# Kernel tuning notes

Measured on AMD Instinct MI355X. Metric: run time of the kernel, lower is better.

The kernel has to match this reference:

```python
import jax, jax.numpy as jnp
import numpy as np

EPS = 1e-6
NUM_HEADS = 16


def _layernorm(x, g, b):
    m = jnp.mean(x, axis=-1, keepdims=True)
    v = jnp.mean(jnp.square(x - m), axis=-1, keepdims=True)
    return (x - m) / jnp.sqrt(v + EPS) * g + b


def _rotate_half(x):
    x1, x2 = jnp.split(x, 2, axis=-1)
    return jnp.concatenate([-x2, x1], axis=-1)


def setup_inputs() -> dict:
    key = jax.random.key(0)
    B, N, C = 2, 2048, 1024
    H = NUM_HEADS
    D = C // H
    F = int(C * 4.0)
    ks = jax.random.split(key, 12)
    s = 0.02
    pos = jnp.arange(N)[:, None].astype(jnp.float32)
    inv_freq = 1.0 / (10000.0 ** (jnp.arange(0, D, 2, dtype=jnp.float32) / D))
    freqs = pos * inv_freq[None, :]          # [N, D/2]
    emb = jnp.concatenate([freqs, freqs], axis=-1)  # [N, D]
    return {
        "x": jax.random.normal(ks[0], (B, N, C), jnp.float32),
        "rotary_cos": jnp.cos(emb),
        "rotary_sin": jnp.sin(emb),
        "ln1_g": jnp.ones((C,), jnp.float32),
        "ln1_b": jnp.zeros((C,), jnp.float32),
        "Wq": jax.random.normal(ks[1], (C, C), jnp.float32) * s,
        "bq": jnp.zeros((C,), jnp.float32),
        "Wk": jax.random.normal(ks[2], (C, C), jnp.float32) * s,
        "bk": jnp.zeros((C,), jnp.float32),
        "Wv": jax.random.normal(ks[3], (C, C), jnp.float32) * s,
        "bv": jnp.zeros((C,), jnp.float32),
        "Wo": jax.random.normal(ks[4], (C, C), jnp.float32) * s,
        "bo": jnp.zeros((C,), jnp.float32),
        "ln2_g": jnp.ones((C,), jnp.float32),
        "ln2_b": jnp.zeros((C,), jnp.float32),
        "W1": jax.random.normal(ks[5], (F, C), jnp.float32) * s,
        "b1": jnp.zeros((F,), jnp.float32),
        "W2": jax.random.normal(ks[6], (C, F), jnp.float32) * s,
        "b2": jnp.zeros((C,), jnp.float32),
    }


def reference(x, rotary_cos, rotary_sin, ln1_g, ln1_b, Wq, bq, Wk, bk, Wv, bv,
              Wo, bo, ln2_g, ln2_b, W1, b1, W2, b2):
    B, N, C = x.shape
    H = NUM_HEADS
    D = C // H

    # --- attention branch ---
    h = _layernorm(x, ln1_g, ln1_b)
    q = (h @ Wq.T + bq).reshape(B, N, H, D).transpose(0, 2, 1, 3)  # [B,H,N,D]
    k = (h @ Wk.T + bk).reshape(B, N, H, D).transpose(0, 2, 1, 3)
    v = (h @ Wv.T + bv).reshape(B, N, H, D).transpose(0, 2, 1, 3)

    cos = rotary_cos[None, None, :, :]  # [1,1,N,D]
    sin = rotary_sin[None, None, :, :]
    q = q * cos + _rotate_half(q) * sin
    k = k * cos + _rotate_half(k) * sin

    scale = D ** -0.5
    attn = jnp.einsum('bhnd,bhmd->bhnm', q, k) * scale
    attn = jax.nn.softmax(attn, axis=-1)
    out = jnp.einsum('bhnm,bhmd->bhnd', attn, v)
    out = out.transpose(0, 2, 1, 3).reshape(B, N, C)
    out = out @ Wo.T + bo
    x = x + out

    # --- MLP branch ---
    h = _layernorm(x, ln2_g, ln2_b)
    h = jax.nn.gelu(h @ W1.T + b1, approximate=False)  # torch nn.GELU exact
    h = h @ W2.T + b2
    return x + h
```

## Files before the change

kernel.cpp:

```cpp
#include <hip/hip_runtime.h>
#include <hip/hip_bf16.h>

#define B_ 2
#define N_ 2048
#define C_ 1024
#define H_ 16
#define D_ 64
#define F_ 4096
#define M_ 4096

typedef __attribute__((ext_vector_type(8))) short bf16x8;
typedef __attribute__((ext_vector_type(4))) float f32x4;

__device__ inline unsigned short f2bf(float f) {
  unsigned int u = __float_as_uint(f);
  u = (u + 0x7FFFu + ((u >> 16) & 1u)) >> 16;
  return (unsigned short)u;
}
__device__ inline float bf2f(unsigned short u) {
  unsigned int x = ((unsigned int)u) << 16;
  return __uint_as_float(x);
}

__global__ __launch_bounds__(256)
void cvt_all(const float4* __restrict__ s0, const float4* __restrict__ s1,
             const float4* __restrict__ s2, const float4* __restrict__ s3,
             const float4* __restrict__ s4, const float4* __restrict__ s5,
             ushort4* __restrict__ d0, ushort4* __restrict__ d1,
             ushort4* __restrict__ d2, ushort4* __restrict__ d3,
             ushort4* __restrict__ d4, ushort4* __restrict__ d5) {
  int b = blockIdx.x;
  const float4* s; ushort4* d; int i;
  if      (b < 1024) { s = s0; d = d0; i = b * 256 + threadIdx.x; }
  else if (b < 2048) { s = s1; d = d1; i = (b - 1024) * 256 + threadIdx.x; }
  else if (b < 3072) { s = s2; d = d2; i = (b - 2048) * 256 + threadIdx.x; }
  else if (b < 4096) { s = s3; d = d3; i = (b - 3072) * 256 + threadIdx.x; }
  else if (b < 8192) { s = s4; d = d4; i = (b - 4096) * 256 + threadIdx.x; }
  else               { s = s5; d = d5; i = (b - 8192) * 256 + threadIdx.x; }
  float4 f = s[i];
  ushort4 o;
  o.x = f2bf(f.x); o.y = f2bf(f.y); o.z = f2bf(f.z); o.w = f2bf(f.w);
  d[i] = o;
}

__global__ __launch_bounds__(256)
void ln_kernel(const float* __restrict__ x, const float* __restrict__ g,
               const float* __restrict__ b, unsigned short* __restrict__ out) {
  __shared__ float red[8];
  const int row = blockIdx.x;
  const int t = threadIdx.x;
  const float4 xv = *(const float4*)(x + row * 1024 + t * 4);
  float s  = xv.x + xv.y + xv.z + xv.w;
  float sq = xv.x * xv.x + xv.y * xv.y + xv.z * xv.z + xv.w * xv.w;
  #pragma unroll
  for (int off = 32; off >= 1; off >>= 1) {
    s  += __shfl_down(s, off);
    sq += __shfl_down(sq, off);
  }
  const int lane = t & 63, wave = t >> 6;
  if (lane == 0) { red[wave * 2] = s; red[wave * 2 + 1] = sq; }
  __syncthreads();
  float ts = red[0] + red[2] + red[4] + red[6];
  float tq = red[1] + red[3] + red[5] + red[7];
  float mean = ts * (1.0f / 1024.0f);
  float var  = tq * (1.0f / 1024.0f) - mean * mean;
  float rstd = rsqrtf(var + 1e-6f);
  float xs[4] = {xv.x, xv.y, xv.z, xv.w};
  #pragma unroll
  for (int i = 0; i < 4; i++) {
    int c = t * 4 + i;
    float y = (xs[i] - mean) * rstd * g[c] + b[c];
    out[row * 1024 + c] = f2bf(y);
  }
}

template<int MODE, int BN>
__global__ __launch_bounds__(256)
void gemm_bt(const unsigned short* __restrict__ A,
             const unsigned short* __restrict__ Bw,
             int K, int Nout, int npc,
             const float* __restrict__ bias,
             const float* __restrict__ resid,
             unsigned short* __restrict__ out_bf,
             float* __restrict__ out_f32) {
  constexpr int NJ = BN / 32;
  __shared__ unsigned short sA[2][128 * 64];
  __shared__ unsigned short sB[2][BN * 64];
  const int t = threadIdx.x;
  const int wave = t >> 6, lane = t & 63;
  const int quad = lane >> 4, l16 = lane & 15;
  const int wm = (wave & 1) * 64, wn = (wave >> 1) * (BN / 2);
  const int id = blockIdx.y * gridDim.x + blockIdx.x;
  const int xcd = id & 7, r_ = id >> 3;
  const int m_blk = xcd * 4 + (r_ & 3);
  const int n_blk = r_ >> 2;
  const int m0 = m_blk * 128, n0 = n_blk * BN;

  f32x4 acc[4][NJ];
  #pragma unroll
  for (int i = 0; i < 4; i++)
    #pragma unroll
    for (int j = 0; j < NJ; j++) acc[i][j] = (f32x4){0.f, 0.f, 0.f, 0.f};

  const int sc = (((t & 7) ^ ((t >> 3) & 7)) * 8);
  const unsigned short* gA = A  + (m0 + (t >> 3)) * K + sc;
  const unsigned short* gB = Bw + (n0 + (t >> 3)) * K + sc;

  auto stage = [&](int k0, int buf) {
    unsigned short* lA = &sA[buf][(wave * 8) * 64];
    unsigned short* lB = &sB[buf][(wave * 8) * 64];
    #pragma unroll
    for (int i = 0; i < 4; i++)
      __builtin_amdgcn_global_load_lds((const unsigned int*)(gA + (32 * i) * K + k0),
                                       (unsigned int*)(lA + 32 * i * 64), 16, 0, 0);
    #pragma unroll
    for (int i = 0; i < BN / 32; i++)
      __builtin_amdgcn_global_load_lds((const unsigned int*)(gB + (32 * i) * K + k0),
                                       (unsigned int*)(lB + 32 * i * 64), 16, 0, 0);
  };

  stage(0, 0);
  __syncthreads();

  const int so0 = ((quad ^ (l16 & 7)) * 8);
  const int so1 = (((4 + quad) ^ (l16 & 7)) * 8);

  const int nk = K >> 6;
  for (int kt = 0; kt < nk; kt++) {
    const int cur = kt & 1;
    if (kt + 1 < nk) stage((kt + 1) * 64, cur ^ 1);
    #pragma unroll
    for (int kk = 0; kk < 2; kk++) {
      const int so = kk ? so1 : so0;
      bf16x8 af[4], bfr[NJ];
      #pragma unroll
      for (int i = 0; i < 4; i++)
        af[i] = *(const bf16x8*)(&sA[cur][(wm + i * 16 + l16) * 64 + so]);
      #pragma unroll
      for (int j = 0; j < NJ; j++)
        bfr[j] = *(const bf16x8*)(&sB[cur][(wn + j * 16 + l16) * 64 + so]);
      #pragma unroll
      for (int i = 0; i < 4; i++)
        #pragma unroll
        for (int j = 0; j < NJ; j++)
          acc[i][j] = __builtin_amdgcn_mfma_f32_16x16x32_bf16(af[i], bfr[j], acc[i][j], 0, 0, 0);
    }
    __syncthreads();
  }

  #pragma unroll
  for (int i = 0; i < 4; i++) {
    #pragma unroll
    for (int j = 0; j < NJ; j++) {
      int col = n0 + wn + j * 16 + l16;
      #pragma unroll
      for (int r = 0; r < 4; r++) {
        int row = m0 + wm + i * 16 + quad * 4 + r;
        float v = acc[i][j][r];
        if (MODE == 1 || MODE == 3) {
          out_f32[row * Nout + col] = v + bias[col] + resid[row * Nout + col];
        } else {
          v += bias[col];
          float w = v * (1.0f + 0.044715f * v * v);
          float gl = v / (1.0f + __expf(-1.5957691216f * w));
          out_bf[row * Nout + col] = f2bf(gl);
        }
      }
    }
  }
}

template<int EPI>
__global__ __launch_bounds__(512, 1)
void gemm256(const unsigned short* __restrict__ A,
             const unsigned short* __restrict__ Bw,
             const float* __restrict__ bias,
             const float* __restrict__ bq, const float* __restrict__ bk,
             const float* __restrict__ bv,
             const float* __restrict__ rc, const float* __restrict__ rs,
             unsigned short* __restrict__ o0,
             unsigned short* __restrict__ ko, unsigned short* __restrict__ vt) {
  const int K = 1024;
  __shared__ unsigned short sA[2][256 * 64];
  __shared__ unsigned short sB[2][256 * 64];
  const int t = threadIdx.x;
  const int wave = t >> 6, lane = t & 63;
  const int quad = lane >> 4, l16 = lane & 15;
  const int wm = (wave & 1) * 128, wn = (wave >> 1) * 64;
  const int id = blockIdx.x;
  const int xcd = id & 7, r_ = id >> 3;
  int m_blk, n_blk;
  if (EPI == 0) { n_blk = xcd * 2 + (r_ >> 4); m_blk = r_ & 15; }
  else          { m_blk = xcd * 2 + r_ / 12;   n_blk = r_ % 12; }
  const int m0 = m_blk * 256, n0 = n_blk * 256;

  f32x4 acc[8][4];
  #pragma unroll
  for (int i = 0; i < 8; i++)
    #pragma unroll
    for (int j = 0; j < 4; j++) acc[i][j] = (f32x4){0.f, 0.f, 0.f, 0.f};

  const int sc = (((t & 7) ^ ((t >> 3) & 7)) * 8);
  const unsigned short* gA = A  + (m0 + (t >> 3)) * K + sc;
  const unsigned short* gB = Bw + (n0 + (t >> 3)) * K + sc;

  auto stage_pair = [&](int k0, int buf, int pr) {
    if (pr < 2) {
      unsigned short* lA = &sA[buf][(wave * 8) * 64];
      #pragma unroll
      for (int r = pr * 2; r < pr * 2 + 2; r++)
        __builtin_amdgcn_global_load_lds((const unsigned int*)(gA + (64 * r) * K + k0),
                                         (unsigned int*)(lA + 64 * r * 64), 16, 0, 0);
    } else {
      unsigned short* lB = &sB[buf][(wave * 8) * 64];
      #pragma unroll
      for (int r = (pr - 2) * 2; r < (pr - 2) * 2 + 2; r++)
        __builtin_amdgcn_global_load_lds((const unsigned int*)(gB + (64 * r) * K + k0),
                                         (unsigned int*)(lB + 64 * r * 64), 16, 0, 0);
    }
  };

  stage_pair(0, 0, 0); stage_pair(0, 0, 1); stage_pair(0, 0, 2); stage_pair(0, 0, 3);
  stage_pair(64, 1, 0);
  asm volatile("s_waitcnt vmcnt(2)" ::: "memory");
  __builtin_amdgcn_s_barrier();

  const int so0 = ((quad ^ (l16 & 7)) * 8);
  const int so1 = (((4 + quad) ^ (l16 & 7)) * 8);

  const int nk = K >> 6;
  for (int t_ = 0; t_ < nk; t_++) {
    const int R = t_ & 1;
    const unsigned short* rA = sA[R];
    const unsigned short* rB = sB[R];
    #pragma unroll
    for (int p = 0; p < 4; p++) {
      const int kk = p >> 1, ih = p & 1;
      const int so = kk ? so1 : so0;
      bf16x8 af[4], bfr[4];
      #pragma unroll
      for (int ii = 0; ii < 4; ii++)
        af[ii] = *(const bf16x8*)(&rA[(wm + (ih * 4 + ii) * 16 + l16) * 64 + so]);
      #pragma unroll
      for (int j = 0; j < 4; j++)
        bfr[j] = *(const bf16x8*)(&rB[(wn + j * 16 + l16) * 64 + so]);
      if (p < 3 && t_ + 1 < nk) stage_pair((t_ + 1) * 64, R ^ 1, p + 1);
      __builtin_amdgcn_s_barrier();
      asm volatile("s_waitcnt lgkmcnt(0)" ::: "memory");
      __builtin_amdgcn_sched_barrier(0);
      __builtin_amdgcn_s_setprio(1);
      #pragma unroll
      for (int ii = 0; ii < 4; ii++)
        #pragma unroll
        for (int j = 0; j < 4; j++)
          acc[ih * 4 + ii][j] =
              __builtin_amdgcn_mfma_f32_16x16x32_bf16(af[ii], bfr[j], acc[ih * 4 + ii][j], 0, 0, 0);
      __builtin_amdgcn_s_setprio(0);
      if (p < 3) __builtin_amdgcn_s_barrier();
    }
    __builtin_amdgcn_s_barrier();
    if (t_ + 2 < nk) {
      stage_pair((t_ + 2) * 64, R, 0);
      asm volatile("s_waitcnt vmcnt(2)" ::: "memory");
      __builtin_amdgcn_s_barrier();
    } else if (t_ + 1 < nk) {
      asm volatile("s_waitcnt vmcnt(0)" ::: "memory");
      __builtin_amdgcn_s_barrier();
    }
  }

  if (EPI == 0) {
    #pragma unroll
    for (int i = 0; i < 8; i++) {
      #pragma unroll
      for (int j = 0; j < 4; j++) {
        int col = n0 + wn + j * 16 + l16;
        float bb = bias[col];
        #pragma unroll
        for (int r = 0; r < 4; r++) {
          int row = m0 + wm + i * 16 + quad * 4 + r;
          float v = acc[i][j][r] + bb;
          float w = v * (1.0f + 0.044715f * v * v);
          float gl = v / (1.0f + __expf(-1.5957691216f * w));
          o0[row * 4096 + col] = f2bf(gl);
        }
      }
    }
  } else {
    const int rgn = n_blk >> 2;
    const int c0 = (n_blk & 3) * 256;
    if (rgn == 2) {
      #pragma unroll
      for (int i = 0; i < 8; i++) {
        int row0 = m0 + wm + i * 16 + quad * 4;
        int bidx = row0 >> 11, n0r = row0 & 2047;
        #pragma unroll
        for (int j = 0; j < 4; j++) {
          int d = j * 16 + l16;
          int c = c0 + wn + d;
          int h = c >> 6;
          float bb = bv[c];
          __hip_bfloat162 p01 = __float22bfloat162_rn(float2{acc[i][j][0] + bb, acc[i][j][1] + bb});
          __hip_bfloat162 p23 = __float22bfloat162_rn(float2{acc[i][j][2] + bb, acc[i][j][3] + bb});
          unsigned int u01, u23;
          __builtin_memcpy(&u01, &p01, 4);
          __builtin_memcpy(&u23, &p23, 4);
          *(uint2*)(vt + (((bidx * 16 + h) * 64) + d) * 2048 + n0r) = make_uint2(u01, u23);
        }
      }
    } else {
      const float* bia = (rgn == 0) ? bq : bk;
      unsigned short* outp = (rgn == 0) ? o0 : ko;
      #pragma unroll
      for (int i = 0; i < 8; i++) {
        #pragma unroll
        for (int r = 0; r < 4; r++) {
          int row = m0 + wm + i * 16 + quad * 4 + r;
          int bidx = row >> 11, n = row & 2047;
          #pragma unroll
          for (int j = 0; j < 4; j++) {
            int d = j * 16 + l16;
            int c = c0 + wn + d;
            int h = c >> 6;
            int oi = ((bidx * 16 + h) * 2048 + n) * 64 + d;
            float val = acc[i][j][r] + bia[c];
            float pv  = acc[i][j ^ 2][r] + bia[c ^ 32];
            float rot = (j < 2) ? -pv : pv;
            float y = val * rc[n * 64 + d] + rot * rs[n * 64 + d];
            if (rgn == 0) y *= 0.125f;
            outp[oi] = f2bf(y);
          }
        }
      }
    }
  }
}

__global__ __launch_bounds__(512)
void flash_attn(const unsigned short* __restrict__ q,
                const unsigned short* __restrict__ k,
                const unsigned short* __restrict__ vt,
                unsigned short* __restrict__ o0h,
                unsigned short* __restrict__ o1h,
                float* __restrict__ l0g, float* __restrict__ l1g) {
  __shared__ unsigned short sK[2][64 * 64];
  __shared__ unsigned short sVt[2][64 * 64];
  __shared__ unsigned short sPt[2][8][16 * 72];
  const int t = threadIdx.x;
  const int wave = t >> 6, lane = t & 63;
  const int quad = lane >> 4, l16 = lane & 15;
  const int id = blockIdx.x;
  const int bh = (id & 7) * 4 + ((id >> 3) & 3);
  const int qb = (id >> 5) & 7;
  const int kvh = id >> 8;
  const int base = bh * (N_ * D_);

  bf16x8 qa[2][2];
  #pragma unroll
  for (int qt = 0; qt < 2; qt++) {
    int qrow = qb * 256 + wave * 32 + qt * 16 + l16;
    #pragma unroll
    for (int kk = 0; kk < 2; kk++)
      qa[qt][kk] = *(const bf16x8*)(q + base + qrow * D_ + kk * 32 + quad * 8);
  }
  float l_i[2] = {0.f, 0.f};
  f32x4 o_acc[2][4];
  #pragma unroll
  for (int qt = 0; qt < 2; qt++)
    #pragma unroll
    for (int dt = 0; dt < 4; dt++) o_acc[qt][dt] = (f32x4){0.f, 0.f, 0.f, 0.f};

  const int sc = (((t & 7) ^ ((t >> 3) & 7)) * 8);
  const unsigned short* gK  = k  + base + (t >> 3) * 64 + sc;
  const unsigned short* gVt = vt + bh * (64 * 2048) + (t >> 3) * 2048 + sc;

  auto stage = [&](int kt, int buf) {
    __builtin_amdgcn_global_load_lds((const unsigned int*)(gK + kt * 64 * 64),
                                     (unsigned int*)(&sK[buf][(wave * 8) * 64]), 16, 0, 0);
    __builtin_amdgcn_global_load_lds((const unsigned int*)(gVt + kt * 64),
                                     (unsigned int*)(&sVt[buf][(wave * 8) * 64]), 16, 0, 0);
  };
  const int kt0 = kvh * 16, kt1 = kt0 + 16;
  stage(kt0, 0);
  __syncthreads();

  const int so0 = ((quad ^ (l16 & 7)) * 8);
  const int so1 = (((4 + quad) ^ (l16 & 7)) * 8);

  for (int kt = kt0; kt < kt1; kt++) {
    const int cur = kt & 1;
    if (kt + 1 < kt1) stage(kt + 1, cur ^ 1);

    f32x4 s_acc[2][4];
    #pragma unroll
    for (int nt = 0; nt < 4; nt++) {
      bf16x8 kb0 = *(const bf16x8*)(&sK[cur][(nt * 16 + l16) * 64 + so0]);
      bf16x8 kb1 = *(const bf16x8*)(&sK[cur][(nt * 16 + l16) * 64 + so1]);
      #pragma unroll
      for (int qt = 0; qt < 2; qt++) {
        f32x4 a = (f32x4){0.f, 0.f, 0.f, 0.f};
        a = __builtin_amdgcn_mfma_f32_16x16x32_bf16(kb0, qa[qt][0], a, 0, 0, 0);
        a = __builtin_amdgcn_mfma_f32_16x16x32_bf16(kb1, qa[qt][1], a, 0, 0, 0);
        s_acc[qt][nt] = a;
      }
    }
    #pragma unroll
    for (int qt = 0; qt < 2; qt++) {
      float rsum = 0.f;
      #pragma unroll
      for (int nt = 0; nt < 4; nt++)
        #pragma unroll
        for (int r = 0; r < 4; r++) {
          float p = __expf(s_acc[qt][nt][r]);
          s_acc[qt][nt][r] = p;
          rsum += p;
        }
      rsum += __shfl_xor(rsum, 16);
      rsum += __shfl_xor(rsum, 32);
      l_i[qt] += rsum;
      #pragma unroll
      for (int nt = 0; nt < 4; nt++) {
        __hip_bfloat162 p01 = __float22bfloat162_rn(float2{s_acc[qt][nt][0], s_acc[qt][nt][1]});
        __hip_bfloat162 p23 = __float22bfloat162_rn(float2{s_acc[qt][nt][2], s_acc[qt][nt][3]});
        unsigned int u01, u23;
        __builtin_memcpy(&u01, &p01, 4);
        __builtin_memcpy(&u23, &p23, 4);
        *(uint2*)(&sPt[qt][wave][l16 * 72 + nt * 16 + quad * 4]) = make_uint2(u01, u23);
      }
    }
    __asm__ volatile("s_waitcnt lgkmcnt(0)" ::: "memory");
    bf16x8 pt[2][2];
    #pragma unroll
    for (int qt = 0; qt < 2; qt++) {
      pt[qt][0] = *(const bf16x8*)(&sPt[qt][wave][l16 * 72 + quad * 8]);
      pt[qt][1] = *(const bf16x8*)(&sPt[qt][wave][l16 * 72 + 32 + quad * 8]);
    }
    #pragma unroll
    for (int dt = 0; dt < 4; dt++) {
      int d0 = dt * 16 + l16;
      bf16x8 va0 = *(const bf16x8*)(&sVt[cur][d0 * 64 + so0]);
      bf16x8 va1 = *(const bf16x8*)(&sVt[cur][d0 * 64 + so1]);
      #pragma unroll
      for (int qt = 0; qt < 2; qt++) {
        o_acc[qt][dt] = __builtin_amdgcn_mfma_f32_16x16x32_bf16(va0, pt[qt][0], o_acc[qt][dt], 0, 0, 0);
        o_acc[qt][dt] = __builtin_amdgcn_mfma_f32_16x16x32_bf16(va1, pt[qt][1], o_acc[qt][dt], 0, 0, 0);
      }
    }
    __syncthreads();
  }

  unsigned short* op = kvh ? o1h : o0h;
  float* lp = kvh ? l1g : l0g;
  const int b = bh >> 4, h = bh & 15;
  #pragma unroll
  for (int qt = 0; qt < 2; qt++) {
    const int qrow = qb * 256 + wave * 32 + qt * 16 + l16;
    if (quad == 0) lp[bh * 2048 + qrow] = l_i[qt];
    const int tok = b * N_ + qrow;
    #pragma unroll
    for (int dt = 0; dt < 4; dt++) {
      __hip_bfloat162 p01 = __float22bfloat162_rn(float2{o_acc[qt][dt][0], o_acc[qt][dt][1]});
      __hip_bfloat162 p23 = __float22bfloat162_rn(float2{o_acc[qt][dt][2], o_acc[qt][dt][3]});
      unsigned int u01, u23;
      __builtin_memcpy(&u01, &p01, 4);
      __builtin_memcpy(&u23, &p23, 4);
      int col = h * 64 + dt * 16 + quad * 4;
      *(uint2*)(op + tok * C_ + col) = make_uint2(u01, u23);
    }
  }
}

__global__ __launch_bounds__(256)
void attn_norm(const unsigned short* __restrict__ o0h,
               const unsigned short* __restrict__ o1h,
               const float* __restrict__ l0g, const float* __restrict__ l1g,
               unsigned short* __restrict__ o) {
  const int i = (blockIdx.x * 256 + threadIdx.x) * 8;
  const int row = i >> 10, c = i & 1023;
  const int h = c >> 6;
  const int b = row >> 11, n = row & 2047;
  const int li = (b * 16 + h) * 2048 + n;
  const float inv = 1.0f / (l0g[li] + l1g[li]);
  ushort4 a0 = *(const ushort4*)(o0h + i);
  ushort4 a1 = *(const ushort4*)(o0h + i + 4);
  ushort4 b0 = *(const ushort4*)(o1h + i);
  ushort4 b1 = *(const ushort4*)(o1h + i + 4);
  ushort4 r0, r1;
  r0.x = f2bf((bf2f(a0.x) + bf2f(b0.x)) * inv);
  r0.y = f2bf((bf2f(a0.y) + bf2f(b0.y)) * inv);
  r0.z = f2bf((bf2f(a0.z) + bf2f(b0.z)) * inv);
  r0.w = f2bf((bf2f(a0.w) + bf2f(b0.w)) * inv);
  r1.x = f2bf((bf2f(a1.x) + bf2f(b1.x)) * inv);
  r1.y = f2bf((bf2f(a1.y) + bf2f(b1.y)) * inv);
  r1.z = f2bf((bf2f(a1.z) + bf2f(b1.z)) * inv);
  r1.w = f2bf((bf2f(a1.w) + bf2f(b1.w)) * inv);
  *(ushort4*)(o + i) = r0;
  *(ushort4*)(o + i + 4) = r1;
}

extern "C" void kernel_launch(void* const* d_in, const int* in_sizes, int n_in,
                              void* d_out, int out_size, void* d_ws, size_t ws_size,
                              hipStream_t stream) {
  const float* x   = (const float*)d_in[0];
  const float* rc  = (const float*)d_in[1];
  const float* rs  = (const float*)d_in[2];
  const float* g1  = (const float*)d_in[3];
  const float* be1 = (const float*)d_in[4];
  const float* Wq  = (const float*)d_in[5];
  const float* bq  = (const float*)d_in[6];
  const float* Wk  = (const float*)d_in[7];
  const float* bk  = (const float*)d_in[8];
  const float* Wv  = (const float*)d_in[9];
  const float* bv  = (const float*)d_in[10];
  const float* Wo  = (const float*)d_in[11];
  const float* bo  = (const float*)d_in[12];
  const float* g2  = (const float*)d_in[13];
  const float* be2 = (const float*)d_in[14];
  const float* W1  = (const float*)d_in[15];
  const float* b1m = (const float*)d_in[16];
  const float* W2  = (const float*)d_in[17];
  const float* b2m = (const float*)d_in[18];
  float* out = (float*)d_out;

  char* ws = (char*)d_ws;
  unsigned short* wqkv = (unsigned short*)(ws + 0);
  unsigned short* wo   = (unsigned short*)(ws + 6291456);
  unsigned short* w1   = (unsigned short*)(ws + 8388608);
  unsigned short* w2   = (unsigned short*)(ws + 16777216);
  unsigned short* h1   = (unsigned short*)(ws + 25165824);
  unsigned short* qa   = (unsigned short*)(ws + 33554432);
  unsigned short* ka   = (unsigned short*)(ws + 41943040);
  unsigned short* va   = (unsigned short*)(ws + 50331648);
  unsigned short* ao   = (unsigned short*)(ws + 58720256);
  float*          x1   = (float*)(ws + 67108864);
  float*          l0   = (float*)(ws + 67108864);
  float*          l1   = l0 + 65536;
  unsigned short* u    = (unsigned short*)(ws + 33554432);

  cvt_all<<<12288, 256, 0, stream>>>(
      (const float4*)Wq, (const float4*)Wk, (const float4*)Wv, (const float4*)Wo,
      (const float4*)W1, (const float4*)W2,
      (ushort4*)wqkv, (ushort4*)(wqkv + 1048576), (ushort4*)(wqkv + 2097152),
      (ushort4*)wo, (ushort4*)w1, (ushort4*)w2);

  ln_kernel<<<4096, 256, 0, stream>>>(x, g1, be1, h1);
  gemm256<1><<<192, 512, 0, stream>>>(h1, wqkv, nullptr, bq, bk, bv, rc, rs, qa, ka, va);
  flash_attn<<<512, 512, 0, stream>>>(qa, ka, va, ao, h1, l0, l1);
  attn_norm<<<2048, 256, 0, stream>>>(ao, h1, l0, l1, ao);
  gemm_bt<1, 64><<<dim3(16, 32), 256, 0, stream>>>(ao, wo, 1024, 1024, 2, bo, x, nullptr, x1);
  ln_kernel<<<4096, 256, 0, stream>>>(x1, g2, be2, h1);
  gemm256<0><<<256, 512, 0, stream>>>(h1, w1, b1m, nullptr, nullptr, nullptr, nullptr, nullptr,
                                      u, nullptr, nullptr);
  gemm_bt<3, 64><<<dim3(16, 32), 256, 0, stream>>>(u, w2, 4096, 1024, 2, b2m, x1, nullptr, out);
}
```

Measured before the change: 375.6 us.

## Replace Wo and W2 GEMMs with split-K 256x128 GEMM using atomic accumulation

The 128x64-tile gemm_bt used for the Wo and W2 projections is replaced by a 256x128-tile, 512-thread split-K kernel. It has a finer-grained staged pipeline with explicit barriers, waitcnt and setprio, and writes results with float atomic adds into an output buffer. That buffer is pre-filled by a separate add_bias kernel holding residual plus bias. The aim is larger tiles for more data reuse and enough blocks to fill the GPU on the K=4096 GEMM. The cost is two extra elementwise launches, atomic traffic in the epilogue, and a summation order that is no longer deterministic.

```diff
diff --git a/kernel.cpp b/kernel.cpp
--- a/kernel.cpp
+++ b/kernel.cpp
@@ -74,97 +74,136 @@
   }
 }
 
-template<int MODE, int BN>
 __global__ __launch_bounds__(256)
-void gemm_bt(const unsigned short* __restrict__ A,
-             const unsigned short* __restrict__ Bw,
-             int K, int Nout, int npc,
-             const float* __restrict__ bias,
-             const float* __restrict__ resid,
-             unsigned short* __restrict__ out_bf,
-             float* __restrict__ out_f32) {
-  constexpr int NJ = BN / 32;
-  __shared__ unsigned short sA[2][128 * 64];
-  __shared__ unsigned short sB[2][BN * 64];
+void add_bias(const float* __restrict__ resid, const float* __restrict__ bias,
+              float* __restrict__ out) {
+  const int i = (blockIdx.x * 256 + threadIdx.x) * 4;
+  const int col = i & 1023;
+  float4 r = *(const float4*)(resid + i);
+  float4 b = *(const float4*)(bias + col);
+  float4 o;
+  o.x = r.x + b.x; o.y = r.y + b.y; o.z = r.z + b.z; o.w = r.w + b.w;
+  *(float4*)(out + i) = o;
+}
+
+__global__ __launch_bounds__(512, 1)
+void gemm_splitk(const unsigned short* __restrict__ A,
+                 const unsigned short* __restrict__ Bw,
+                 int Kfull, int ksplit,
+                 float* __restrict__ out) {
+  __shared__ unsigned short sA[2][256 * 64];
+  __shared__ unsigned short sB[2][128 * 64];
   const int t = threadIdx.x;
   const int wave = t >> 6, lane = t & 63;
   const int quad = lane >> 4, l16 = lane & 15;
-  const int wm = (wave & 1) * 64, wn = (wave >> 1) * (BN / 2);
-  const int id = blockIdx.y * gridDim.x + blockIdx.x;
+  const int wm = (wave >> 1) * 64, wn = (wave & 1) * 64;
+  const int id = blockIdx.x;
   const int xcd = id & 7, r_ = id >> 3;
-  const int m_blk = xcd * 4 + (r_ & 3);
-  const int n_blk = r_ >> 2;
-  const int m0 = m_blk * 128, n0 = n_blk * BN;
-
-  f32x4 acc[4][NJ];
+  const int m_blk = xcd * 2 + (r_ & 1);
+  const int cu = r_ >> 1;
+  const int n_blk = cu & 7;
+  const int split = cu >> 3;
+  const int m0 = m_blk * 256, n0 = n_blk * 128;
+  const int k0base = split * ksplit;
+
+  f32x4 acc[4][4];
   #pragma unroll
   for (int i = 0; i < 4; i++)
     #pragma unroll
-    for (int j = 0; j < NJ; j++) acc[i][j] = (f32x4){0.f, 0.f, 0.f, 0.f};
+    for (int j = 0; j < 4; j++) acc[i][j] = (f32x4){0.f, 0.f, 0.f, 0.f};
 
   const int sc = (((t & 7) ^ ((t >> 3) & 7)) * 8);
-  const unsigned short* gA = A  + (m0 + (t >> 3)) * K + sc;
-  const unsigned short* gB = Bw + (n0 + (t >> 3)) * K + sc;
-
-  auto stage = [&](int k0, int buf) {
-    unsigned short* lA = &sA[buf][(wave * 8) * 64];
-    unsigned short* lB = &sB[buf][(wave * 8) * 64];
-    #pragma unroll
-    for (int i = 0; i < 4; i++)
-      __builtin_amdgcn_global_load_lds((const unsigned int*)(gA + (32 * i) * K + k0),
-                                       (unsigned int*)(lA + 32 * i * 64), 16, 0, 0);
-    #pragma unroll
-    for (int i = 0; i < BN / 32; i++)
-      __builtin_amdgcn_global_load_lds((const unsigned int*)(gB + (32 * i) * K + k0),
-                                       (unsigned int*)(lB + 32 * i * 64), 16, 0, 0);
+  const unsigned short* gA = A  + (long)(m0 + (t >> 3)) * Kfull + k0base + sc;
+  const unsigned short* gB = Bw + (long)(n0 + (t >> 3)) * Kfull + k0base + sc;
+
+  auto stage_pair = [&](int k0, int buf, int pr) {
+    if (pr < 2) {
+      #pragma unroll
+      for (int i = pr * 2; i < pr * 2 + 2; i++)
+        __builtin_amdgcn_global_load_lds((const unsigned int*)(gA + (long)(64 * i) * Kfull + k0),
+                                         (unsigned int*)(&sA[buf][i * 4096 + wave * 8 * 64]), 16, 0, 0);
+    } else {
+      #pragma unroll
+      for (int i = 0; i < 2; i++)
+        __builtin_amdgcn_global_load_lds((const unsigned int*)(gB + (long)(64 * i) * Kfull + k0),
+                                         (unsigned int*)(&sB[buf][i * 4096 + wave * 8 * 64]), 16, 0, 0);
+    }
   };
 
-  stage(0, 0);
-  __syncthreads();
+  stage_pair(0, 0, 0); stage_pair(0, 0, 1); stage_pair(0, 0, 2);
+  stage_pair(64, 1, 0);
+  asm volatile("s_waitcnt vmcnt(2)" ::: "memory");
+  __builtin_amdgcn_s_barrier();
 
   const int so0 = ((quad ^ (l16 & 7)) * 8);
   const int so1 = (((4 + quad) ^ (l16 & 7)) * 8);
 
-  const int nk = K >> 6;
-  for (int kt = 0; kt < nk; kt++) {
-    const int cur = kt & 1;
-    if (kt + 1 < nk) stage((kt + 1) * 64, cur ^ 1);
-    #pragma unroll
-    for (int kk = 0; kk < 2; kk++) {
-      const int so = kk ? so1 : so0;
-      bf16x8 af[4], bfr[NJ];
-      #pragma unroll
-      for (int i = 0; i < 4; i++)
-        af[i] = *(const bf16x8*)(&sA[cur][(wm + i * 16 + l16) * 64 + so]);
-      #pragma unroll
-      for (int j = 0; j < NJ; j++)
-        bfr[j] = *(const bf16x8*)(&sB[cur][(wn + j * 16 + l16) * 64 + so]);
-      #pragma unroll
-      for (int i = 0; i < 4; i++)
-        #pragma unroll
-        for (int j = 0; j < NJ; j++)
-          acc[i][j] = __builtin_amdgcn_mfma_f32_16x16x32_bf16(af[i], bfr[j], acc[i][j], 0, 0, 0);
-    }
-    __syncthreads();
-  }
-
-  #pragma unroll
-  for (int i = 0; i < 4; i++) {
-    #pragma unroll
-    for (int j = 0; j < NJ; j++) {
+  const int nk = ksplit >> 6;
+  for (int t_ = 0; t_ < nk; t_++) {
+    const int R = t_ & 1;
+    const unsigned short* rA = sA[R];
+    const unsigned short* rB = sB[R];
+    {
+      bf16x8 af[4], bfr[4];
+      #pragma unroll
+      for (int ii = 0; ii < 4; ii++)
+        af[ii] = *(const bf16x8*)(&rA[(wm + ii * 16 + l16) * 64 + so0]);
+      #pragma unroll
+      for (int j = 0; j < 4; j++)
+        bfr[j] = *(const bf16x8*)(&rB[(wn + j * 16 + l16) * 64 + so0]);
+      if (t_ + 1 < nk) stage_pair((t_ + 1) * 64, R ^ 1, 1);
+      __builtin_amdgcn_s_barrier();
+      asm volatile("s_waitcnt lgkmcnt(0)" ::: "memory");
+      __builtin_amdgcn_sched_barrier(0);
+      __builtin_amdgcn_s_setprio(1);
+      #pragma unroll
+      for (int ii = 0; ii < 4; ii++)
+        #pragma unroll
+        for (int j = 0; j < 4; j++)
+          acc[ii][j] = __builtin_amdgcn_mfma_f32_16x16x32_bf16(af[ii], bfr[j], acc[ii][j], 0, 0, 0);
+      __builtin_amdgcn_s_setprio(0);
+      __builtin_amdgcn_s_barrier();
+    }
+    {
+      bf16x8 af[4], bfr[4];
+      #pragma unroll
+      for (int ii = 0; ii < 4; ii++)
+        af[ii] = *(const bf16x8*)(&rA[(wm + ii * 16 + l16) * 64 + so1]);
+      #pragma unroll
+      for (int j = 0; j < 4; j++)
+        bfr[j] = *(const bf16x8*)(&rB[(wn + j * 16 + l16) * 64 + so1]);
+      if (t_ + 1 < nk) stage_pair((t_ + 1) * 64, R ^ 1, 2);
+      __builtin_amdgcn_s_barrier();
+      asm volatile("s_waitcnt lgkmcnt(0)" ::: "memory");
+      __builtin_amdgcn_sched_barrier(0);
+      __builtin_amdgcn_s_setprio(1);
+      #pragma unroll
+      for (int ii = 0; ii < 4; ii++)
+        #pragma unroll
+        for (int j = 0; j < 4; j++)
+          acc[ii][j] = __builtin_amdgcn_mfma_f32_16x16x32_bf16(af[ii], bfr[j], acc[ii][j], 0, 0, 0);
+      __builtin_amdgcn_s_setprio(0);
+    }
+    __builtin_amdgcn_s_barrier();
+    if (t_ + 2 < nk) {
+      stage_pair((t_ + 2) * 64, R, 0);
+      asm volatile("s_waitcnt vmcnt(2)" ::: "memory");
+      __builtin_amdgcn_s_barrier();
+    } else if (t_ + 1 < nk) {
+      asm volatile("s_waitcnt vmcnt(0)" ::: "memory");
+      __builtin_amdgcn_s_barrier();
+    }
+  }
+
+  #pragma unroll
+  for (int ii = 0; ii < 4; ii++) {
+    #pragma unroll
+    for (int j = 0; j < 4; j++) {
       int col = n0 + wn + j * 16 + l16;
       #pragma unroll
       for (int r = 0; r < 4; r++) {
-        int row = m0 + wm + i * 16 + quad * 4 + r;
-        float v = acc[i][j][r];
-        if (MODE == 1 || MODE == 3) {
-          out_f32[row * Nout + col] = v + bias[col] + resid[row * Nout + col];
-        } else {
-          v += bias[col];
-          float w = v * (1.0f + 0.044715f * v * v);
-          float gl = v / (1.0f + __expf(-1.5957691216f * w));
-          out_bf[row * Nout + col] = f2bf(gl);
-        }
+        int row = m0 + wm + ii * 16 + quad * 4 + r;
+        unsafeAtomicAdd(&out[row * 1024 + col], acc[ii][j][r]);
       }
     }
   }
@@ -547,9 +586,11 @@
   gemm256<1><<<192, 512, 0, stream>>>(h1, wqkv, nullptr, bq, bk, bv, rc, rs, qa, ka, va);
   flash_attn<<<512, 512, 0, stream>>>(qa, ka, va, ao, h1, l0, l1);
   attn_norm<<<2048, 256, 0, stream>>>(ao, h1, l0, l1, ao);
-  gemm_bt<1, 64><<<dim3(16, 32), 256, 0, stream>>>(ao, wo, 1024, 1024, 2, bo, x, nullptr, x1);
+  add_bias<<<4096, 256, 0, stream>>>(x, bo, x1);
+  gemm_splitk<<<256, 512, 0, stream>>>(ao, wo, 1024, 512, x1);
   ln_kernel<<<4096, 256, 0, stream>>>(x1, g2, be2, h1);
   gemm256<0><<<256, 512, 0, stream>>>(h1, w1, b1m, nullptr, nullptr, nullptr, nullptr, nullptr,
                                       u, nullptr, nullptr);
-  gemm_bt<3, 64><<<dim3(16, 32), 256, 0, stream>>>(u, w2, 4096, 1024, 2, b2m, x1, nullptr, out);
-}
+  add_bias<<<4096, 256, 0, stream>>>(x1, b2m, out);
+  gemm_splitk<<<256, 512, 0, stream>>>(u, w2, 4096, 2048, out);
+}
```

Measured after the change: 412.4 us. 9.8% more time.
